# Kernel optimization log

Hardware: AMD Instinct MI355X
Metric: run time of the kernel (lower is better)

## Reference

```python
import jax, jax.numpy as jnp
import numpy as np

B, T, I, H = 128, 512, 1024, 1024


def _xavier(key, shape):
    # matches torch nn.init.xavier_uniform_
    fan_in, fan_out = shape
    limit = float(np.sqrt(6.0 / (fan_in + fan_out)))
    return jax.random.uniform(key, shape, jnp.float32, -limit, limit)


def setup_inputs() -> dict:
    key = jax.random.key(0)
    ks = jax.random.split(key, 9)
    x = jax.random.normal(ks[0], (B, T, I), dtype=jnp.float32)
    names = ['W_ii', 'W_hi', 'W_if', 'W_hf', 'W_ig', 'W_hg', 'W_io', 'W_ho']
    inp = {'x': x}
    for k, name in zip(ks[1:], names):
        shape = (I, H) if name[2] == 'i' else (H, H)
        inp[name] = _xavier(k, shape)
    for bname in ['b_ii', 'b_hi', 'b_if', 'b_hf', 'b_ig', 'b_hg', 'b_io', 'b_ho']:
        inp[bname] = jnp.zeros((H,), dtype=jnp.float32)
    return inp


def reference(x, W_ii, b_ii, W_hi, b_hi, W_if, b_if, W_hf, b_hf,
              W_ig, b_ig, W_hg, b_hg, W_io, b_io, W_ho, b_ho):
    """LSTM over x [B, T, I]; returns final (h_t, c_t), each [B, H].
    Faithful to the module's per-gate math (input gate i, forget gate f,
    cell candidate g with tanh, output gate o with sigmoid), zero init state.
    Gates are fused into one input GEMM per step group: precompute x @ W_i*
    for all timesteps at once, then scan the recurrence."""
    batch, seq, _ = x.shape
    hidden = W_hi.shape[0]
    # Precompute input projections for all timesteps: [T, B, 4H]
    W_in = jnp.concatenate([W_ii, W_if, W_ig, W_io], axis=1)          # [I, 4H]
    b_in = jnp.concatenate([b_ii + b_hi, b_if + b_hf, b_ig + b_hg, b_io + b_ho])
    x_proj = jnp.einsum('bti,ih->tbh', x, W_in) + b_in                # [T, B, 4H]
    W_h = jnp.concatenate([W_hi, W_hf, W_hg, W_ho], axis=1)           # [H, 4H]

    def step(carry, xp):
        h, c = carry
        gates = xp + h @ W_h                                          # [B, 4H]
        i_t = jax.nn.sigmoid(gates[:, 0 * hidden:1 * hidden])
        f_t = jax.nn.sigmoid(gates[:, 1 * hidden:2 * hidden])
        g_t = jnp.tanh(gates[:, 2 * hidden:3 * hidden])
        o_t = jax.nn.sigmoid(gates[:, 3 * hidden:4 * hidden])
        c = f_t * c + i_t * g_t
        h = o_t * jnp.tanh(c)
        return (h, c), None

    h0 = jnp.zeros((batch, hidden), dtype=x.dtype)
    c0 = jnp.zeros((batch, hidden), dtype=x.dtype)
    (h_t, c_t), _ = jax.lax.scan(step, (h0, c0), x_proj)
    return (h_t, c_t)
```

## Files before the change

kernel.cpp:

```cpp
#include <hip/hip_runtime.h>
#include <cstdint>
#include <cstddef>


#define B_  128
#define T_  512
#define I_  1024
#define H_  1024
#define G4_ 4096
#define SLOTG 32768ull

typedef __attribute__((ext_vector_type(8))) short short8;
typedef __attribute__((ext_vector_type(4))) float f32x4;
typedef __attribute__((ext_vector_type(2))) unsigned long long u64x2;
typedef unsigned long long u64;

static __device__ __forceinline__ unsigned short f2bf(float f) {
    unsigned u = __builtin_bit_cast(unsigned, f);
    u += 0x7fffu + ((u >> 16) & 1u);
    return (unsigned short)(u >> 16);
}
static __device__ __forceinline__ float bf2f(unsigned short s) {
    unsigned u = (unsigned)s << 16;
    return __builtin_bit_cast(float, u);
}
static __device__ __forceinline__ float sigm(float x) {
    return 1.0f / (1.0f + exp2f(-1.4426950408889634f * x));
}
static __device__ __forceinline__ float tanh_(float x) {
    float e = exp2f(2.8853900817779268f * x);
    return 1.0f - 2.0f / (e + 1.0f);
}
static __device__ __forceinline__ f32x4 mfma16(short8 a, short8 b, f32x4 c) {
    return __builtin_amdgcn_mfma_f32_16x16x32_bf16(a, b, c, 0, 0, 0);
}
static __device__ __forceinline__ u64 ffbits(u64 v) {
    return ((~v) - 0x0001000100010001ull) & v & 0x8000800080008000ull;
}
#define AL(p)    __hip_atomic_load((p), __ATOMIC_RELAXED, __HIP_MEMORY_SCOPE_AGENT)
#define ARMW(p)  __hip_atomic_fetch_add((p), 0ull, __ATOMIC_RELAXED, __HIP_MEMORY_SCOPE_AGENT)
#define ARMW32(p) __hip_atomic_fetch_add((p), 0u, __ATOMIC_RELAXED, __HIP_MEMORY_SCOPE_AGENT)

__global__ __launch_bounds__(256) void pack_w8(
    const float* w0, const float* w1, const float* w2, const float* w3,
    const float* w4, const float* w5, const float* w6, const float* w7,
    unsigned short* __restrict__ Winp, unsigned short* __restrict__ Whp) {
    const float* ws[8] = {w0, w1, w2, w3, w4, w5, w6, w7};
    const float* W = ws[blockIdx.z];
    unsigned short* dst = (blockIdx.z < 4) ? Winp : Whp;
    const int g = blockIdx.z & 3;
    __shared__ float tile[64][65];
    const int tid = threadIdx.x;
    const int k0 = blockIdx.y * 64;
    const int j0 = blockIdx.x * 64;
    {
        const int r  = tid >> 2;
        const int c0 = (tid & 3) * 16;
        const float* src = W + (size_t)(k0 + r) * H_ + j0 + c0;
        #pragma unroll
        for (int q = 0; q < 4; ++q) {
            float4 v = *(const float4*)(src + q * 4);
            tile[r][c0 + q*4 + 0] = v.x;
            tile[r][c0 + q*4 + 1] = v.y;
            tile[r][c0 + q*4 + 2] = v.z;
            tile[r][c0 + q*4 + 3] = v.w;
        }
    }
    __syncthreads();
    {
        const int jl   = tid >> 2;
        const int kseg = (tid & 3) * 16;
        unsigned short* orow = dst + ((size_t)(j0 + jl) * 4 + g) * 1024 + (k0 + kseg);
        #pragma unroll
        for (int q = 0; q < 16; q += 4) {
            ushort4 u;
            u.x = f2bf(tile[kseg + q + 0][jl]);
            u.y = f2bf(tile[kseg + q + 1][jl]);
            u.z = f2bf(tile[kseg + q + 2][jl]);
            u.w = f2bf(tile[kseg + q + 3][jl]);
            *(ushort4*)(orow + q) = u;
        }
    }
}

__global__ __launch_bounds__(256) void pack_bias(
    const float* b0x, const float* b0h, const float* b1x, const float* b1h,
    const float* b2x, const float* b2h, const float* b3x, const float* b3h,
    float* __restrict__ out) {
    int jc = blockIdx.x * 256 + threadIdx.x;
    int g = jc & 3, jh = jc >> 2;
    const float* bx = (g == 0) ? b0x : (g == 1) ? b1x : (g == 2) ? b2x : b3x;
    const float* bh = (g == 0) ? b0h : (g == 1) ? b1h : (g == 2) ? b2h : b3h;
    out[jc] = bx[jh] + bh[jh];
}

__global__ __launch_bounds__(256) void init_cnt(unsigned* __restrict__ cnt, int total) {
    int i = blockIdx.x * 256 + threadIdx.x;
    if (i < total) cnt[i] = (i < 8 * 32 * 16) ? 8u : 0u;
}

__global__ __launch_bounds__(256) void convert_x(const float* __restrict__ x,
                                                 unsigned short* __restrict__ xb,
                                                 int t0, int Tcc) {
    int e = blockIdx.x * 256 + threadIdx.x;
    int i = (e & 127) << 3;
    int r = e >> 7;
    int b = r / Tcc, tc = r - b * Tcc;
    const float* s = x + (size_t)(b * T_ + t0 + tc) * I_ + i;
    float4 v0 = *(const float4*)s;
    float4 v1 = *(const float4*)(s + 4);
    ushort4 u0; u0.x = f2bf(v0.x); u0.y = f2bf(v0.y); u0.z = f2bf(v0.z); u0.w = f2bf(v0.w);
    ushort4 u1; u1.x = f2bf(v1.x); u1.y = f2bf(v1.y); u1.z = f2bf(v1.z); u1.w = f2bf(v1.w);
    unsigned short* d = xb + (size_t)r * I_ + i;
    *(ushort4*)d = u0;
    *(ushort4*)(d + 4) = u1;
}

__global__ __launch_bounds__(256) void gemm_xproj(
    const unsigned short* __restrict__ A,
    const unsigned short* __restrict__ Bt,
    const float* __restrict__ bias,
    unsigned short* __restrict__ xp,
    u64* __restrict__ sent,
    int Tcc) {
    __shared__ unsigned short ot[64][256];
    const int tid = threadIdx.x;
    const int w = tid >> 6, l = tid & 63;
    const int l15 = l & 15, hi = l >> 4;
    const int row0 = blockIdx.y * 64;
    const int col0 = blockIdx.x * 256 + w * 64;
    f32x4 acc[4][4] = {};
    const unsigned short* a0 = A  + (size_t)(row0 + l15) * 1024 + hi * 8;
    const unsigned short* b0 = Bt + (size_t)(col0 + l15) * 1024 + hi * 8;
    for (int ks = 0; ks < 1024; ks += 32) {
        short8 a[4], bb[4];
        #pragma unroll
        for (int mi = 0; mi < 4; ++mi) a[mi]  = *(const short8*)(a0 + (size_t)mi * 16 * 1024 + ks);
        #pragma unroll
        for (int ni = 0; ni < 4; ++ni) bb[ni] = *(const short8*)(b0 + (size_t)ni * 16 * 1024 + ks);
        #pragma unroll
        for (int mi = 0; mi < 4; ++mi)
            #pragma unroll
            for (int ni = 0; ni < 4; ++ni)
                acc[mi][ni] = mfma16(a[mi], bb[ni], acc[mi][ni]);
    }
    #pragma unroll
    for (int mi = 0; mi < 4; ++mi) {
        #pragma unroll
        for (int ni = 0; ni < 4; ++ni) {
            float bs = bias[col0 + ni * 16 + l15];
            #pragma unroll
            for (int j = 0; j < 4; ++j)
                ot[mi * 16 + hi * 4 + j][w * 64 + ni * 16 + l15] =
                    f2bf(acc[mi][ni][j] + bs);
        }
    }
    __syncthreads();
    {
        const int rl = tid >> 2, ch = tid & 3;
        int r = row0 + rl;
        int b = r / Tcc, tc = r - b * Tcc;
        unsigned short* dst = xp + (size_t)(tc * 128 + b) * G4_
                            + blockIdx.x * 256 + ch * 64;
        const unsigned short* src = &ot[rl][ch * 64];
        #pragma unroll
        for (int q = 0; q < 8; ++q)
            *(uint4*)(dst + q * 8) = *(const uint4*)(src + q * 8);
    }
    {
        size_t bid = (size_t)blockIdx.y * 16 + blockIdx.x;
        u64* sp = sent + bid * 1024 + (size_t)tid * 4;
        sp[0] = ~0ull; sp[1] = ~0ull; sp[2] = ~0ull; sp[3] = ~0ull;
    }
}

__global__ __launch_bounds__(1024, 4) void lstm_recur(
    const unsigned short* __restrict__ Whp,
    const unsigned short* __restrict__ xp,
    u64* __restrict__ hring,
    unsigned* __restrict__ cnt,
    float* __restrict__ cbuf,
    float* __restrict__ outp,
    int Tcc, int t0, int is_last) {
    __shared__ __align__(16) char hlds[32768];
    __shared__ __align__(16) float gl[4][16][132];

    const int t = threadIdx.x;
    const int l = t & 63, w = t >> 6;
    const int l15 = l & 15, hi = l >> 4;
    const int cq = w & 3, kq = w >> 2;
    const int grp = blockIdx.x >> 5, cb = blockIdx.x & 31;
    const int row0 = grp * 16;

    short8 wf[2][8];
    {
        const unsigned short* wb = Whp + (size_t)(cb * 128 + cq * 32 + l15) * 1024
                                       + kq * 256 + hi * 8;
        #pragma unroll
        for (int ci = 0; ci < 2; ++ci)
            #pragma unroll
            for (int ks = 0; ks < 8; ++ks)
                wf[ci][ks] = *(const short8*)(wb + ci * 16 * 1024 + ks * 32);
    }

    const int urow = t >> 5, ujh = t & 31;
    float creg = 0.f;
    if (t < 512) creg = cbuf[(size_t)(row0 + urow) * H_ + cb * 32 + ujh];

    const int arow = t & 15, ach = t >> 4;

    for (int st = 0; st < Tcc; ++st) {
        ushort4 xv = {0, 0, 0, 0};
        if (t < 512)
            xv = *(const ushort4*)(xp + ((size_t)st * 128 + row0 + urow) * G4_
                                      + cb * 128 + ujh * 4);

        if (w == 0) {
            unsigned* fp = cnt + (((size_t)(t0 + st) * 8 + grp) * 32 + l) * 16;
            for (;;) {
                unsigned v = 8u;
                if (l < 32) v = ARMW32(fp);
                if (__all(v >= 8u)) break;
                __builtin_amdgcn_s_sleep(1);
            }
        }
        __syncthreads();

        {
            u64* rp = hring + (size_t)st * SLOTG + (size_t)(row0 + arow) * 256 + ach * 4;
            u64 q0 = AL(rp), q1 = AL(rp + 1), q2 = AL(rp + 2), q3 = AL(rp + 3);
            while (ffbits(q0) | ffbits(q1) | ffbits(q2) | ffbits(q3)) {
                __builtin_amdgcn_s_sleep(1);
                q0 = ARMW(rp); q1 = ARMW(rp + 1); q2 = ARMW(rp + 2); q3 = ARMW(rp + 3);
            }
            u64x2 v0 = {q0, q1}, v1 = {q2, q3};
            *(u64x2*)(hlds + ((ach * 2    ) * 16 + arow) * 16) = v0;
            *(u64x2*)(hlds + ((ach * 2 + 1) * 16 + arow) * 16) = v1;
        }
        __syncthreads();

        f32x4 acc[2] = {};
        #pragma unroll
        for (int ks = 0; ks < 8; ++ks) {
            int ko = (kq * 8 + ks) * 4 + hi;
            short8 a = *(const short8*)(hlds + ko * 256 + l15 * 16);
            acc[0] = mfma16(a, wf[0][ks], acc[0]);
            acc[1] = mfma16(a, wf[1][ks], acc[1]);
        }
        #pragma unroll
        for (int ci = 0; ci < 2; ++ci)
            #pragma unroll
            for (int j = 0; j < 4; ++j)
                gl[kq][hi * 4 + j][cq * 32 + ci * 16 + l15] = acc[ci][j];
        __syncthreads();

        if (t < 512) {
            float4 s = *(const float4*)&gl[0][urow][ujh * 4];
            #pragma unroll
            for (int k2 = 1; k2 < 4; ++k2) {
                float4 s2 = *(const float4*)&gl[k2][urow][ujh * 4];
                s.x += s2.x; s.y += s2.y; s.z += s2.z; s.w += s2.w;
            }
            float gi = s.x + bf2f(xv.x);
            float gf = s.y + bf2f(xv.y);
            float gg = s.z + bf2f(xv.z);
            float go = s.w + bf2f(xv.w);
            float it_ = sigm(gi), ft = sigm(gf), gt = tanh_(gg), ot = sigm(go);
            float cn = ft * creg + it_ * gt;
            float hn = ot * tanh_(cn);
            creg = cn;
            unsigned hb = (unsigned)f2bf(hn);
            unsigned ob = __shfl_xor(hb, 1);
            unsigned v01 = (l & 1) ? (ob | (hb << 16)) : (hb | (ob << 16));
            unsigned v23 = __shfl_xor(v01, 2);
            if ((t & 3) == 0) {
                u64 hw = (u64)v01 | ((u64)v23 << 32);
                int dst = (st == Tcc - 1) ? 0 : st + 1;
                u64* wp = hring + (size_t)dst * SLOTG
                        + (size_t)(row0 + urow) * 256 + cb * 8 + (ujh >> 2);
                (void)__hip_atomic_exchange(wp, hw, __ATOMIC_RELAXED,
                                            __HIP_MEMORY_SCOPE_AGENT);
            }
            if (is_last && st == Tcc - 1) {
                size_t o = (size_t)(row0 + urow) * H_ + cb * 32 + ujh;
                outp[o] = hn;
                outp[(size_t)B_ * H_ + o] = cn;
            }
            asm volatile("s_waitcnt vmcnt(0)" ::: "memory");
            if ((t & 63) == 0)
                (void)__hip_atomic_fetch_add(
                    cnt + (((size_t)(t0 + st + 1) * 8 + grp) * 32 + cb) * 16,
                    1u, __ATOMIC_RELAXED, __HIP_MEMORY_SCOPE_AGENT);
        }
    }
    if (t < 512)
        cbuf[(size_t)(row0 + urow) * H_ + cb * 32 + ujh] = creg;
}

extern "C" void kernel_launch(void* const* d_in, const int* in_sizes, int n_in,
                              void* d_out, int out_size, void* d_ws, size_t ws_size,
                              hipStream_t stream) {
    const float* x = (const float*)d_in[0];
    const float* Wx[4] = {(const float*)d_in[1], (const float*)d_in[3],
                          (const float*)d_in[5], (const float*)d_in[7]};
    const float* Wh[4] = {(const float*)d_in[2], (const float*)d_in[4],
                          (const float*)d_in[6], (const float*)d_in[8]};
    const float* bx[4] = {(const float*)d_in[9],  (const float*)d_in[11],
                          (const float*)d_in[13], (const float*)d_in[15]};
    const float* bh[4] = {(const float*)d_in[10], (const float*)d_in[12],
                          (const float*)d_in[14], (const float*)d_in[16]};

    char* p = (char*)d_ws;
    auto take = [&](size_t bytes) {
        char* q = p; p += (bytes + 255) & ~(size_t)255; return q;
    };
    unsigned short* Winp = (unsigned short*)take((size_t)G4_ * 1024 * 2);
    unsigned short* Whp  = (unsigned short*)take((size_t)G4_ * 1024 * 2);
    float*          bias = (float*)take(G4_ * 4);
    float*          cbuf = (float*)take((size_t)B_ * H_ * 4);
    const int cnt_total = (T_ + 1) * 8 * 32 * 16;
    unsigned*       cnt  = (unsigned*)take((size_t)cnt_total * 4);
    size_t fixed = (size_t)(p - (char*)d_ws) + SLOTG * 8 + 512;
    size_t per = (size_t)B_ * I_ * 2 + (size_t)B_ * G4_ * 2 + SLOTG * 8 + 768;
    size_t avail = ws_size > fixed ? ws_size - fixed : 0;
    int Tc = (int)(avail / per);
    if (Tc > T_) Tc = T_;
    if (Tc < 2) Tc = 2;
    unsigned short* xb    = (unsigned short*)take((size_t)Tc * B_ * I_ * 2);
    unsigned short* xpc   = (unsigned short*)take((size_t)Tc * B_ * G4_ * 2);
    u64*            hring = (u64*)take((size_t)(Tc + 1) * SLOTG * 8);

    pack_w8<<<dim3(16, 16, 8), 256, 0, stream>>>(
        Wx[0], Wx[1], Wx[2], Wx[3], Wh[0], Wh[1], Wh[2], Wh[3], Winp, Whp);
    pack_bias<<<16, 256, 0, stream>>>(bx[0], bh[0], bx[1], bh[1],
                                      bx[2], bh[2], bx[3], bh[3], bias);
    init_cnt<<<(cnt_total + 255) / 256, 256, 0, stream>>>(cnt, cnt_total);
    (void)hipMemsetAsync(hring, 0, SLOTG * 8, stream);
    (void)hipMemsetAsync(cbuf, 0, (size_t)B_ * H_ * 4, stream);

    int t0 = 0;
    while (t0 < T_) {
        int rem = T_ - t0;
        int Tcc = (rem < Tc) ? rem : Tc;
        if (rem - Tcc == 1) Tcc -= 1;
        int last = (t0 + Tcc >= T_) ? 1 : 0;
        convert_x<<<Tcc * 64, 256, 0, stream>>>(x, xb, t0, Tcc);
        gemm_xproj<<<dim3(16, 2 * Tcc), 256, 0, stream>>>(
            xb, Winp, bias, xpc, hring + SLOTG, Tcc);
        lstm_recur<<<256, 1024, 0, stream>>>(Whp, xpc, hring, cnt, cbuf,
                                             (float*)d_out, Tcc, t0, last);
        t0 += Tcc;
    }
}
```

Before: 4.558 ms.

## Replace counter barrier with sentinel polling on h ring and remap blocks

Drops the per-step arrival counter array and its spin wait in warp 0. Each consumer thread now polls its own slots in the h ring until the 0xFFFF sentinel halves are gone, so a block can start as soon as the data it needs has arrived. The sentinel fill moves from the gemm epilogue to a memset before each recurrence launch. Block-to-(group, column) mapping is swapped, and the last step skips the ring write. The risk is more global polling traffic and reliance on relaxed atomics for visibility.

```diff
diff --git a/kernel.cpp b/kernel.cpp
--- a/kernel.cpp
+++ b/kernel.cpp
@@ -37,9 +37,8 @@
 static __device__ __forceinline__ u64 ffbits(u64 v) {
     return ((~v) - 0x0001000100010001ull) & v & 0x8000800080008000ull;
 }
-#define AL(p)    __hip_atomic_load((p), __ATOMIC_RELAXED, __HIP_MEMORY_SCOPE_AGENT)
-#define ARMW(p)  __hip_atomic_fetch_add((p), 0ull, __ATOMIC_RELAXED, __HIP_MEMORY_SCOPE_AGENT)
-#define ARMW32(p) __hip_atomic_fetch_add((p), 0u, __ATOMIC_RELAXED, __HIP_MEMORY_SCOPE_AGENT)
+#define AL(p)   __hip_atomic_load((p), __ATOMIC_RELAXED, __HIP_MEMORY_SCOPE_AGENT)
+#define ARMW(p) __hip_atomic_fetch_add((p), 0ull, __ATOMIC_RELAXED, __HIP_MEMORY_SCOPE_AGENT)
 
 __global__ __launch_bounds__(256) void pack_w8(
     const float* w0, const float* w1, const float* w2, const float* w3,
@@ -94,11 +93,6 @@
     out[jc] = bx[jh] + bh[jh];
 }
 
-__global__ __launch_bounds__(256) void init_cnt(unsigned* __restrict__ cnt, int total) {
-    int i = blockIdx.x * 256 + threadIdx.x;
-    if (i < total) cnt[i] = (i < 8 * 32 * 16) ? 8u : 0u;
-}
-
 __global__ __launch_bounds__(256) void convert_x(const float* __restrict__ x,
                                                  unsigned short* __restrict__ xb,
                                                  int t0, int Tcc) {
@@ -121,7 +115,6 @@
     const unsigned short* __restrict__ Bt,
     const float* __restrict__ bias,
     unsigned short* __restrict__ xp,
-    u64* __restrict__ sent,
     int Tcc) {
     __shared__ unsigned short ot[64][256];
     const int tid = threadIdx.x;
@@ -167,21 +160,15 @@
         for (int q = 0; q < 8; ++q)
             *(uint4*)(dst + q * 8) = *(const uint4*)(src + q * 8);
     }
-    {
-        size_t bid = (size_t)blockIdx.y * 16 + blockIdx.x;
-        u64* sp = sent + bid * 1024 + (size_t)tid * 4;
-        sp[0] = ~0ull; sp[1] = ~0ull; sp[2] = ~0ull; sp[3] = ~0ull;
-    }
 }
 
 __global__ __launch_bounds__(1024, 4) void lstm_recur(
     const unsigned short* __restrict__ Whp,
     const unsigned short* __restrict__ xp,
     u64* __restrict__ hring,
-    unsigned* __restrict__ cnt,
     float* __restrict__ cbuf,
     float* __restrict__ outp,
-    int Tcc, int t0, int is_last) {
+    int Tcc, int is_last) {
     __shared__ __align__(16) char hlds[32768];
     __shared__ __align__(16) float gl[4][16][132];
 
@@ -189,7 +176,8 @@
     const int l = t & 63, w = t >> 6;
     const int l15 = l & 15, hi = l >> 4;
     const int cq = w & 3, kq = w >> 2;
-    const int grp = blockIdx.x >> 5, cb = blockIdx.x & 31;
+    const int grp = blockIdx.x & 7;
+    const int cb  = blockIdx.x >> 3;
     const int row0 = grp * 16;
 
     short8 wf[2][8];
@@ -207,7 +195,7 @@
     float creg = 0.f;
     if (t < 512) creg = cbuf[(size_t)(row0 + urow) * H_ + cb * 32 + ujh];
 
-    const int arow = t & 15, ach = t >> 4;
+    const int prow = t & 15, lq = t >> 4;
 
     for (int st = 0; st < Tcc; ++st) {
         ushort4 xv = {0, 0, 0, 0};
@@ -215,27 +203,35 @@
             xv = *(const ushort4*)(xp + ((size_t)st * 128 + row0 + urow) * G4_
                                       + cb * 128 + ujh * 4);
 
-        if (w == 0) {
-            unsigned* fp = cnt + (((size_t)(t0 + st) * 8 + grp) * 32 + l) * 16;
-            for (;;) {
-                unsigned v = 8u;
-                if (l < 32) v = ARMW32(fp);
-                if (__all(v >= 8u)) break;
+        if (t < 512) {
+            u64 q[8];
+            u64* rp = hring + (size_t)st * SLOTG + (size_t)(row0 + prow) * 256 + lq * 8;
+            int it = 0;
+            q[0] = AL(rp);
+            while (ffbits(q[0])) {
+                ++it;
                 __builtin_amdgcn_s_sleep(1);
-            }
-        }
-        __syncthreads();
-
-        {
-            u64* rp = hring + (size_t)st * SLOTG + (size_t)(row0 + arow) * 256 + ach * 4;
-            u64 q0 = AL(rp), q1 = AL(rp + 1), q2 = AL(rp + 2), q3 = AL(rp + 3);
-            while (ffbits(q0) | ffbits(q1) | ffbits(q2) | ffbits(q3)) {
+                q[0] = (it < 64) ? AL(rp) : ARMW(rp);
+            }
+            q[1] = AL(rp + 1); q[2] = AL(rp + 2); q[3] = AL(rp + 3);
+            q[4] = AL(rp + 4); q[5] = AL(rp + 5); q[6] = AL(rp + 6); q[7] = AL(rp + 7);
+            u64 bad = ffbits(q[1]) | ffbits(q[2]) | ffbits(q[3]) | ffbits(q[4])
+                    | ffbits(q[5]) | ffbits(q[6]) | ffbits(q[7]);
+            int it2 = 0;
+            while (bad) {
+                ++it2;
                 __builtin_amdgcn_s_sleep(1);
-                q0 = ARMW(rp); q1 = ARMW(rp + 1); q2 = ARMW(rp + 2); q3 = ARMW(rp + 3);
-            }
-            u64x2 v0 = {q0, q1}, v1 = {q2, q3};
-            *(u64x2*)(hlds + ((ach * 2    ) * 16 + arow) * 16) = v0;
-            *(u64x2*)(hlds + ((ach * 2 + 1) * 16 + arow) * 16) = v1;
+                #pragma unroll
+                for (int j = 1; j < 8; ++j)
+                    if (ffbits(q[j])) q[j] = (it2 < 64) ? AL(rp + j) : ARMW(rp + j);
+                bad = ffbits(q[1]) | ffbits(q[2]) | ffbits(q[3]) | ffbits(q[4])
+                    | ffbits(q[5]) | ffbits(q[6]) | ffbits(q[7]);
+            }
+            #pragma unroll
+            for (int j = 0; j < 4; ++j) {
+                u64x2 v = {q[2 * j], q[2 * j + 1]};
+                *(u64x2*)(hlds + ((lq * 4 + j) * 16 + prow) * 16) = v;
+            }
         }
         __syncthreads();
 
@@ -269,28 +265,25 @@
             float cn = ft * creg + it_ * gt;
             float hn = ot * tanh_(cn);
             creg = cn;
-            unsigned hb = (unsigned)f2bf(hn);
-            unsigned ob = __shfl_xor(hb, 1);
-            unsigned v01 = (l & 1) ? (ob | (hb << 16)) : (hb | (ob << 16));
-            unsigned v23 = __shfl_xor(v01, 2);
-            if ((t & 3) == 0) {
-                u64 hw = (u64)v01 | ((u64)v23 << 32);
-                int dst = (st == Tcc - 1) ? 0 : st + 1;
-                u64* wp = hring + (size_t)dst * SLOTG
-                        + (size_t)(row0 + urow) * 256 + cb * 8 + (ujh >> 2);
-                (void)__hip_atomic_exchange(wp, hw, __ATOMIC_RELAXED,
-                                            __HIP_MEMORY_SCOPE_AGENT);
-            }
             if (is_last && st == Tcc - 1) {
                 size_t o = (size_t)(row0 + urow) * H_ + cb * 32 + ujh;
                 outp[o] = hn;
                 outp[(size_t)B_ * H_ + o] = cn;
-            }
-            asm volatile("s_waitcnt vmcnt(0)" ::: "memory");
-            if ((t & 63) == 0)
-                (void)__hip_atomic_fetch_add(
-                    cnt + (((size_t)(t0 + st + 1) * 8 + grp) * 32 + cb) * 16,
-                    1u, __ATOMIC_RELAXED, __HIP_MEMORY_SCOPE_AGENT);
+            } else {
+                unsigned hb = (unsigned)f2bf(hn);
+                unsigned ob = __shfl_xor(hb, 1);
+                unsigned v01 = (l & 1) ? (ob | (hb << 16)) : (hb | (ob << 16));
+                unsigned v23 = __shfl_xor(v01, 2);
+                if ((t & 3) == 0) {
+                    u64 hw = (u64)v01 | ((u64)v23 << 32);
+                    int dst = (st == Tcc - 1) ? 0 : st + 1;
+                    u64* wp = hring + (size_t)dst * SLOTG
+                            + (size_t)(row0 + urow) * 256 + cb * 8 + (ujh >> 2);
+                    *(volatile u64*)wp = hw;
+                    (void)__hip_atomic_exchange(wp, hw, __ATOMIC_RELAXED,
+                                                __HIP_MEMORY_SCOPE_AGENT);
+                }
+            }
         }
     }
     if (t < 512)
@@ -318,8 +311,6 @@
     unsigned short* Whp  = (unsigned short*)take((size_t)G4_ * 1024 * 2);
     float*          bias = (float*)take(G4_ * 4);
     float*          cbuf = (float*)take((size_t)B_ * H_ * 4);
-    const int cnt_total = (T_ + 1) * 8 * 32 * 16;
-    unsigned*       cnt  = (unsigned*)take((size_t)cnt_total * 4);
     size_t fixed = (size_t)(p - (char*)d_ws) + SLOTG * 8 + 512;
     size_t per = (size_t)B_ * I_ * 2 + (size_t)B_ * G4_ * 2 + SLOTG * 8 + 768;
     size_t avail = ws_size > fixed ? ws_size - fixed : 0;
@@ -334,7 +325,6 @@
         Wx[0], Wx[1], Wx[2], Wx[3], Wh[0], Wh[1], Wh[2], Wh[3], Winp, Whp);
     pack_bias<<<16, 256, 0, stream>>>(bx[0], bh[0], bx[1], bh[1],
                                       bx[2], bh[2], bx[3], bh[3], bias);
-    init_cnt<<<(cnt_total + 255) / 256, 256, 0, stream>>>(cnt, cnt_total);
     (void)hipMemsetAsync(hring, 0, SLOTG * 8, stream);
     (void)hipMemsetAsync(cbuf, 0, (size_t)B_ * H_ * 4, stream);
 
@@ -346,9 +336,11 @@
         int last = (t0 + Tcc >= T_) ? 1 : 0;
         convert_x<<<Tcc * 64, 256, 0, stream>>>(x, xb, t0, Tcc);
         gemm_xproj<<<dim3(16, 2 * Tcc), 256, 0, stream>>>(
-            xb, Winp, bias, xpc, hring + SLOTG, Tcc);
-        lstm_recur<<<256, 1024, 0, stream>>>(Whp, xpc, hring, cnt, cbuf,
-                                             (float*)d_out, Tcc, t0, last);
+            xb, Winp, bias, xpc, Tcc);
+        (void)hipMemsetAsync(hring + SLOTG, 0xFF,
+                             (size_t)Tcc * SLOTG * 8, stream);
+        lstm_recur<<<256, 1024, 0, stream>>>(Whp, xpc, hring, cbuf,
+                                             (float*)d_out, Tcc, last);
         t0 += Tcc;
     }
 }
```

New measurement: 5.518 ms. 21.1% more time.
